# Optimization experiments

Hardware: AMD Instinct MI355X
Metric: run time of the kernel (lower is better)

## Reference

```python
import jax, jax.numpy as jnp
import numpy as np

V, D, H, L, T, B = 50257, 768, 12, 12, 1024, 2
S = 0.02


def setup_inputs() -> dict:
    key = jax.random.key(0)
    ks = jax.random.split(key, 8)
    return {
        "idx": jax.random.randint(ks[0], (B, T), 0, V),
        "wte": jax.random.normal(ks[1], (V, D), jnp.float32) * S,   # tied tok_emb / head
        "pos": jax.random.normal(ks[2], (T, D), jnp.float32) * S,
        "ln1_g": jnp.ones((L, D), jnp.float32),
        "ln1_b": jnp.zeros((L, D), jnp.float32),
        "qkv_w": jax.random.normal(ks[3], (L, D, 3 * D), jnp.float32) * S,
        "qkv_b": jnp.zeros((L, 3 * D), jnp.float32),
        "proj_w": jax.random.normal(ks[4], (L, D, D), jnp.float32) * S,
        "proj_b": jnp.zeros((L, D), jnp.float32),
        "ln2_g": jnp.ones((L, D), jnp.float32),
        "ln2_b": jnp.zeros((L, D), jnp.float32),
        "fc1_w": jax.random.normal(ks[5], (L, D, 4 * D), jnp.float32) * S,
        "fc1_b": jnp.zeros((L, 4 * D), jnp.float32),
        "fc2_w": jax.random.normal(ks[6], (L, 4 * D, D), jnp.float32) * S,
        "fc2_b": jnp.zeros((L, D), jnp.float32),
        "lnf_g": jnp.ones((D,), jnp.float32),
        "lnf_b": jnp.zeros((D,), jnp.float32),
    }


def _ln(x, g, b):
    m = x.mean(-1, keepdims=True)
    v = ((x - m) ** 2).mean(-1, keepdims=True)
    return (x - m) * jax.lax.rsqrt(v + 1e-5) * g + b


def reference(idx, wte, pos, ln1_g, ln1_b, qkv_w, qkv_b, proj_w, proj_b,
              ln2_g, ln2_b, fc1_w, fc1_b, fc2_w, fc2_b, lnf_g, lnf_b):
    b, t = idx.shape
    hd = D // H
    x = wte[idx] + pos[None, :t]                       # [B,T,D]
    causal = jnp.triu(jnp.ones((t, t), bool), 1)       # True above diagonal -> masked

    def block(x, p):
        l1g, l1b, qw, qb, pw, pb, l2g, l2b, f1w, f1b, f2w, f2b = p
        h = _ln(x, l1g, l1b)
        qkv = (h @ qw + qb).reshape(b, t, 3, H, hd).transpose(2, 0, 3, 1, 4)
        q, k, v = qkv[0], qkv[1], qkv[2]               # [B,H,T,hd]
        att = jnp.einsum('bhqd,bhkd->bhqk', q, k) * hd ** -0.5
        att = jnp.where(causal, -jnp.inf, att)
        att = jax.nn.softmax(att, axis=-1)
        o = jnp.einsum('bhqk,bhkd->bhqd', att, v)
        o = o.transpose(0, 2, 1, 3).reshape(b, t, D)
        x = x + o @ pw + pb
        h = _ln(x, l2g, l2b)
        h = jax.nn.gelu(h @ f1w + f1b, approximate=False)
        x = x + h @ f2w + f2b
        return x, None

    x, _ = jax.lax.scan(block, x, (ln1_g, ln1_b, qkv_w, qkv_b, proj_w, proj_b,
                                   ln2_g, ln2_b, fc1_w, fc1_b, fc2_w, fc2_b))
    x = _ln(x, lnf_g, lnf_b)
    return x @ wte.T                                   # tied head -> [B,T,V]
```

## Files before the change

kernel.cpp:

```cpp
#include <hip/hip_runtime.h>
#include <math.h>

#define D 768
#define T 1024
#define BATCH 2
#define NH 12
#define NL 12
#define V 50257
#define NT 2048

typedef _Float16 half4_t __attribute__((ext_vector_type(4)));
typedef _Float16 half8_t __attribute__((ext_vector_type(8)));
typedef float floatx4 __attribute__((ext_vector_type(4)));

__device__ inline float wave_reduce_sum(float v) {
  #pragma unroll
  for (int off = 32; off > 0; off >>= 1) v += __shfl_xor(v, off, 64);
  return v;
}

__device__ __forceinline__ void gld16(const _Float16* g, _Float16* l) {
  __builtin_amdgcn_global_load_lds(
      (const __attribute__((address_space(1))) unsigned int*)g,
      (__attribute__((address_space(3))) unsigned int*)l, 16, 0, 0);
}

__global__ __launch_bounds__(256) void embed_kernel(const int* __restrict__ idx,
    const float* __restrict__ wte, const float* __restrict__ pos,
    float* __restrict__ x) {
  int row = blockIdx.x;
  int tok = idx[row];
  int tp  = row & (T - 1);
  const float* ws = wte + (size_t)tok * D;
  const float* ps = pos + (size_t)tp * D;
  float* xr = x + (size_t)row * D;
  for (int i = threadIdx.x; i < D; i += 256) xr[i] = ws[i] + ps[i];
}

__global__ __launch_bounds__(256) void cvt16_kernel(const float* __restrict__ src,
    _Float16* __restrict__ dst, int n4) {
  int i = blockIdx.x * 256 + threadIdx.x;
  int stride = gridDim.x * 256;
  for (; i < n4; i += stride) {
    float4 v = ((const float4*)src)[i];
    half4_t h;
    h[0] = (_Float16)v.x; h[1] = (_Float16)v.y;
    h[2] = (_Float16)v.z; h[3] = (_Float16)v.w;
    ((half4_t*)dst)[i] = h;
  }
}

__global__ __launch_bounds__(256) void wconv_kernel(
    const float* __restrict__ qkvw, const float* __restrict__ projw,
    const float* __restrict__ fc1w, const float* __restrict__ fc2w,
    _Float16* __restrict__ q16, _Float16* __restrict__ p16,
    _Float16* __restrict__ f116, _Float16* __restrict__ f216) {
  int id = blockIdx.x;
  size_t l = blockIdx.y;
  const float* src; _Float16* dst; int K, N, tn;
  if (id < 1728)      { src = qkvw + l * (D * 3 * D); dst = q16  + l * (2304 * 768); K = 768;  N = 2304; tn = id; }
  else if (id < 2304) { src = projw + l * (D * D);    dst = p16  + l * (768 * 768);  K = 768;  N = 768;  tn = id - 1728; }
  else if (id < 4608) { src = fc1w + l * (D * 4 * D); dst = f116 + l * (3072 * 768); K = 768;  N = 3072; tn = id - 2304; }
  else                { src = fc2w + l * (4 * D * D); dst = f216 + l * (3072 * 768); K = 3072; N = 768;  tn = id - 4608; }
  int ntn = N >> 5;
  int tc = (tn % ntn) * 32;
  int tr = (tn / ntn) * 32;
  __shared__ float tile[32][33];
  int tx = threadIdx.x & 31, ty = threadIdx.x >> 5;
  #pragma unroll
  for (int j = 0; j < 4; ++j)
    tile[ty + 8 * j][tx] = src[(size_t)(tr + ty + 8 * j) * N + tc + tx];
  __syncthreads();
  #pragma unroll
  for (int j = 0; j < 4; ++j)
    dst[(size_t)(tc + ty + 8 * j) * K + tr + tx] = (_Float16)tile[tx][ty + 8 * j];
}

__global__ __launch_bounds__(256) void ln_kernel(const float* __restrict__ x,
    const float* __restrict__ g, const float* __restrict__ bta,
    _Float16* __restrict__ y) {
  const int lane = threadIdx.x & 63, wave = threadIdx.x >> 6;
  const int row = blockIdx.x * 4 + wave;
  const float4* xr = (const float4*)(x + (size_t)row * D);
  half4_t* yr = (half4_t*)(y + (size_t)row * D);

  float4 a[3];
  #pragma unroll
  for (int j = 0; j < 3; ++j) a[j] = xr[lane + 64 * j];

  float s = 0.f;
  #pragma unroll
  for (int j = 0; j < 3; ++j) s += a[j].x + a[j].y + a[j].z + a[j].w;
  float mean = wave_reduce_sum(s) * (1.f / D);

  float v = 0.f;
  #pragma unroll
  for (int j = 0; j < 3; ++j) {
    float dx = a[j].x - mean, dy = a[j].y - mean, dz = a[j].z - mean, dw = a[j].w - mean;
    v += dx * dx + dy * dy + dz * dz + dw * dw;
  }
  float rstd = rsqrtf(wave_reduce_sum(v) * (1.f / D) + 1e-5f);

  #pragma unroll
  for (int j = 0; j < 3; ++j) {
    float4 gg = ((const float4*)g)[lane + 64 * j];
    float4 bb = ((const float4*)bta)[lane + 64 * j];
    half4_t h;
    h[0] = (_Float16)((a[j].x - mean) * rstd * gg.x + bb.x);
    h[1] = (_Float16)((a[j].y - mean) * rstd * gg.y + bb.y);
    h[2] = (_Float16)((a[j].z - mean) * rstd * gg.z + bb.z);
    h[3] = (_Float16)((a[j].w - mean) * rstd * gg.w + bb.w);
    yr[lane + 64 * j] = h;
  }
}

__global__ __launch_bounds__(256) void attn_kernel(
    const _Float16* __restrict__ qkv,
    const _Float16* __restrict__ vt,
    _Float16* __restrict__ o) {
  const int qt   = (int)gridDim.x - 1 - (int)blockIdx.x;
  const int h    = blockIdx.y;
  const int b    = blockIdx.z;
  const int tid  = threadIdx.x;
  const int lane = tid & 63, wave = tid >> 6;
  const int lr = lane & 15, g = lane >> 4;
  const int lk = g * 8;
  const int cr = g * 4;

  __shared__ __align__(16) _Float16 Ks[2][2][64][32];
  __shared__ __align__(16) _Float16 Vs[2][2][64][32];
  __shared__ __align__(16) _Float16 Pl[4][16][72];

  const int RS = 3 * D;
  const int q0 = qt * 64 + wave * 16;

  const _Float16* qrow = qkv + (size_t)(b * T + q0 + lr) * RS + h * 64;
  half8_t aq0 = *(const half8_t*)(qrow + lk);
  half8_t aq1 = *(const half8_t*)(qrow + 32 + lk);
  #pragma unroll
  for (int j = 0; j < 8; ++j) { aq0[j] *= (_Float16)0.125f; aq1[j] *= (_Float16)0.125f; }

  const int sr = wave * 16 + (lane >> 2);
  const int sc = (lane & 3) * 8;
  const _Float16* ksrc = qkv + (size_t)(b * T + sr) * RS + D + h * 64 + sc;
  const _Float16* vsrc = vt + (size_t)((b * NH + h) * 64 + sr) * T + sc;

#define ASTAGE(bufn, kk) do {                                   \
    const _Float16* kp_ = ksrc + (size_t)((kk) * 64) * RS;      \
    gld16(kp_,      &Ks[bufn][0][wave * 16][0]);                \
    gld16(kp_ + 32, &Ks[bufn][1][wave * 16][0]);                \
    gld16(vsrc + (kk) * 64,      &Vs[bufn][0][wave * 16][0]);   \
    gld16(vsrc + (kk) * 64 + 32, &Vs[bufn][1][wave * 16][0]);   \
  } while (0)

  floatx4 oa[4] = {};
  float m_r[4] = {-1e30f, -1e30f, -1e30f, -1e30f};
  float l_r[4] = {0.f, 0.f, 0.f, 0.f};

  ASTAGE(0, 0);
  __syncthreads();

  for (int kt = 0; kt <= qt; ++kt) {
    const int cur = kt & 1;
    if (kt < qt) ASTAGE(cur ^ 1, kt + 1);

    floatx4 s4[4];
    #pragma unroll
    for (int kc = 0; kc < 4; ++kc) {
      half8_t bk0 = *(const half8_t*)&Ks[cur][0][kc * 16 + lr][lk];
      half8_t bk1 = *(const half8_t*)&Ks[cur][1][kc * 16 + lr][lk];
      floatx4 z = {};
      z = __builtin_amdgcn_mfma_f32_16x16x32_f16(aq0, bk0, z, 0, 0, 0);
      z = __builtin_amdgcn_mfma_f32_16x16x32_f16(aq1, bk1, z, 0, 0, 0);
      s4[kc] = z;
    }
    if (kt == qt) {
      #pragma unroll
      for (int kc = 0; kc < 4; ++kc)
        #pragma unroll
        for (int i = 0; i < 4; ++i)
          if (kc * 16 + lr > wave * 16 + cr + i) s4[kc][i] = -1e30f;
    }

    float alpha[4], psum[4];
    #pragma unroll
    for (int i = 0; i < 4; ++i) {
      float v = fmaxf(fmaxf(s4[0][i], s4[1][i]), fmaxf(s4[2][i], s4[3][i]));
      #pragma unroll
      for (int off = 1; off < 16; off <<= 1) v = fmaxf(v, __shfl_xor(v, off, 64));
      float mn = fmaxf(m_r[i], v);
      alpha[i] = __expf(m_r[i] - mn);
      m_r[i] = mn;
      psum[i] = 0.f;
    }
    #pragma unroll
    for (int kc = 0; kc < 4; ++kc)
      #pragma unroll
      for (int i = 0; i < 4; ++i) {
        float p = __expf(s4[kc][i] - m_r[i]);
        psum[i] += p;
        Pl[wave][cr + i][kc * 16 + lr] = (_Float16)p;
      }
    #pragma unroll
    for (int i = 0; i < 4; ++i) {
      float s = psum[i];
      #pragma unroll
      for (int off = 1; off < 16; off <<= 1) s += __shfl_xor(s, off, 64);
      l_r[i] = l_r[i] * alpha[i] + s;
    }
    #pragma unroll
    for (int dc = 0; dc < 4; ++dc)
      #pragma unroll
      for (int i = 0; i < 4; ++i) oa[dc][i] *= alpha[i];

    half8_t ap0 = *(const half8_t*)&Pl[wave][lr][lk];
    half8_t ap1 = *(const half8_t*)&Pl[wave][lr][32 + lk];
    #pragma unroll
    for (int dc = 0; dc < 4; ++dc) {
      half8_t bv0 = *(const half8_t*)&Vs[cur][0][dc * 16 + lr][lk];
      half8_t bv1 = *(const half8_t*)&Vs[cur][1][dc * 16 + lr][lk];
      oa[dc] = __builtin_amdgcn_mfma_f32_16x16x32_f16(ap0, bv0, oa[dc], 0, 0, 0);
      oa[dc] = __builtin_amdgcn_mfma_f32_16x16x32_f16(ap1, bv1, oa[dc], 0, 0, 0);
    }
    __syncthreads();
  }
#undef ASTAGE

  _Float16* orow = o + (size_t)(b * T + q0) * D + h * 64;
  #pragma unroll
  for (int i = 0; i < 4; ++i) {
    float inv = 1.f / l_r[i];
    #pragma unroll
    for (int dc = 0; dc < 4; ++dc)
      orow[(size_t)(cr + i) * D + dc * 16 + lr] = (_Float16)(oa[dc][i] * inv);
  }
}

template <bool GELU, bool VT, bool ATOMIC, bool NTS, typename OutT>
__global__ __launch_bounds__(256) void gemm16_kernel(
    const _Float16* __restrict__ A, const _Float16* __restrict__ Bt,
    const float* __restrict__ bias, const float* __restrict__ res,
    OutT* __restrict__ C, _Float16* __restrict__ vt, int M, int N, int K) {
  __shared__ __align__(16) char smem_raw[33792];
  _Float16 (*As)[128][32] = (_Float16(*)[128][32])smem_raw;
  _Float16 (*Bs)[128][32] = (_Float16(*)[128][32])(smem_raw + 16384);

  const int t = threadIdx.x;
  const int lane = t & 63, wave = t >> 6;

  const int gx = gridDim.x, gy = gridDim.y;
  const int nwg = gx * gy;
  int f = blockIdx.y * gx + blockIdx.x;
  int id = (f & 7) * (nwg >> 3) + (f >> 3);
  const int n0 = (id / gy) * 128;
  const int m0 = (id % gy) * 128;

  const int ks = K / gridDim.z;
  const int kbeg = blockIdx.z * ks, kend = kbeg + ks;

  const int wm = (wave >> 1) * 64, wn = (wave & 1) * 64;
  const int lr = lane & 15;
  const int lk = (lane >> 4) * 8;

  const int srow = lane >> 2;
  const int scol = (lane & 3) * 8;
  const _Float16* a_src0 = A + (size_t)(m0 + wave * 32 + srow) * K + scol;
  const _Float16* a_src1 = a_src0 + (size_t)16 * K;
  const int bn0 = min(n0 + wave * 32 + srow, N - 1);
  const int bn1 = min(n0 + wave * 32 + 16 + srow, N - 1);
  const _Float16* b_src0 = Bt + (size_t)bn0 * K + scol;
  const _Float16* b_src1 = Bt + (size_t)bn1 * K + scol;

#define GSTAGE(bufn, kk) do {                            \
    gld16(a_src0 + (kk), &As[bufn][wave * 32][0]);       \
    gld16(a_src1 + (kk), &As[bufn][wave * 32 + 16][0]);  \
    gld16(b_src0 + (kk), &Bs[bufn][wave * 32][0]);       \
    gld16(b_src1 + (kk), &Bs[bufn][wave * 32 + 16][0]);  \
  } while (0)

  floatx4 acc[4][4] = {};

  GSTAGE(0, kbeg);
  __syncthreads();

  const int nIter = (kend - kbeg) >> 5;
  for (int i = 0; i < nIter; ++i) {
    const int cur = i & 1;
    if (i + 1 < nIter) GSTAGE(cur ^ 1, kbeg + ((i + 1) << 5));

    half8_t af[4], bb[4];
    #pragma unroll
    for (int mi = 0; mi < 4; ++mi)
      af[mi] = *(const half8_t*)&As[cur][wm + mi * 16 + lr][lk];
    #pragma unroll
    for (int ni = 0; ni < 4; ++ni)
      bb[ni] = *(const half8_t*)&Bs[cur][wn + ni * 16 + lr][lk];
    #pragma unroll
    for (int mi = 0; mi < 4; ++mi)
      #pragma unroll
      for (int ni = 0; ni < 4; ++ni)
        acc[mi][ni] = __builtin_amdgcn_mfma_f32_16x16x32_f16(
            af[mi], bb[ni], acc[mi][ni], 0, 0, 0);
    __syncthreads();
  }
#undef GSTAGE

  const int cr = (lane >> 4) * 4;

  if (NTS) {
    float (*ob)[132] = (float(*)[132])smem_raw;
    #pragma unroll
    for (int h2 = 0; h2 < 2; ++h2) {
      __syncthreads();
      if ((wave >> 1) == h2) {
        #pragma unroll
        for (int mi = 0; mi < 4; ++mi)
          #pragma unroll
          for (int ni = 0; ni < 4; ++ni) {
            floatx4 v = acc[mi][ni];
            #pragma unroll
            for (int i = 0; i < 4; ++i)
              ob[mi * 16 + cr + i][wn + ni * 16 + lr] = v[i];
          }
      }
      __syncthreads();
      const int col = t & 127;
      const int n = n0 + col;
      if (n < N) {
        #pragma unroll
        for (int r2 = 0; r2 < 32; ++r2) {
          int rloc = r2 * 2 + (t >> 7);
          int m = m0 + h2 * 64 + rloc;
          __builtin_nontemporal_store((OutT)ob[rloc][col], &C[(size_t)m * N + n]);
        }
      }
    }
    return;
  }

  #pragma unroll
  for (int mi = 0; mi < 4; ++mi) {
    #pragma unroll
    for (int ni = 0; ni < 4; ++ni) {
      int n = n0 + wn + ni * 16 + lr;
      if (n >= N) continue;
      floatx4 v = acc[mi][ni];
      float bs = (bias && (!ATOMIC || blockIdx.z == 0)) ? bias[n] : 0.f;
      if (VT && n >= 2 * D) {
        int d  = n - 2 * D;
        int mb = m0 + wm + mi * 16 + cr;
        half4_t h4;
        #pragma unroll
        for (int i = 0; i < 4; ++i) h4[i] = (_Float16)(v[i] + bs);
        *(half4_t*)(vt + ((size_t)((mb >> 10) * NH + (d >> 6)) * 64 + (d & 63)) * T
                       + (mb & 1023)) = h4;
      } else if (ATOMIC) {
        #pragma unroll
        for (int i = 0; i < 4; ++i) {
          int m = m0 + wm + mi * 16 + cr + i;
          atomicAdd((float*)&C[(size_t)m * N + n], v[i] + bs);
        }
      } else {
        #pragma unroll
        for (int i = 0; i < 4; ++i) {
          int m = m0 + wm + mi * 16 + cr + i;
          float vv = v[i] + bs;
          if (res)  vv += res[(size_t)m * N + n];
          if (GELU) vv = 0.5f * vv * (1.f + erff(vv * 0.70710678118f));
          C[(size_t)m * N + n] = (OutT)vv;
        }
      }
    }
  }
}

extern "C" void kernel_launch(void* const* d_in, const int* in_sizes, int n_in,
                              void* d_out, int out_size, void* d_ws, size_t ws_size,
                              hipStream_t stream) {
  const int*   idx   = (const int*)d_in[0];
  const float* wte   = (const float*)d_in[1];
  const float* pos   = (const float*)d_in[2];
  const float* ln1g  = (const float*)d_in[3];
  const float* ln1b  = (const float*)d_in[4];
  const float* qkvw  = (const float*)d_in[5];
  const float* qkvb  = (const float*)d_in[6];
  const float* projw = (const float*)d_in[7];
  const float* projb = (const float*)d_in[8];
  const float* ln2g  = (const float*)d_in[9];
  const float* ln2b  = (const float*)d_in[10];
  const float* fc1w  = (const float*)d_in[11];
  const float* fc1b  = (const float*)d_in[12];
  const float* fc2w  = (const float*)d_in[13];
  const float* fc2b  = (const float*)d_in[14];
  const float* lnfg  = (const float*)d_in[15];
  const float* lnfb  = (const float*)d_in[16];
  float* out = (float*)d_out;

  float* ws = (float*)d_ws;
  float* x = ws;
  _Float16* big16  = (_Float16*)(x + (size_t)NT * D);
  _Float16* vt16   = big16 + (size_t)NT * 4 * D;
  _Float16* hbuf16 = vt16 + (size_t)BATCH * NH * 64 * T;
  _Float16* obuf16 = hbuf16 + (size_t)NT * D;
  _Float16* wte16  = obuf16 + (size_t)NT * D;
  _Float16* wbase  = wte16 + (size_t)V * D;

  const size_t QSZ = (size_t)2304 * 768, PSZ = (size_t)768 * 768;
  const size_t F1SZ = (size_t)3072 * 768, F2SZ = (size_t)3072 * 768;
  const size_t PERL = QSZ + PSZ + F1SZ + F2SZ;
  const size_t fixed_bytes = (char*)wbase - (char*)d_ws;
  const bool all12 = ws_size >= fixed_bytes + 12 * PERL * sizeof(_Float16);
  const int nlw = all12 ? 12 : 1;

  _Float16* q16  = wbase;
  _Float16* p16  = q16  + QSZ * nlw;
  _Float16* f116 = p16  + PSZ * nlw;
  _Float16* f216 = f116 + F1SZ * nlw;

  cvt16_kernel<<<2048, 256, 0, stream>>>(wte, wte16, (V * D) / 4);
  embed_kernel<<<NT, 256, 0, stream>>>(idx, wte, pos, x);
  if (all12)
    wconv_kernel<<<dim3(6912, 12), 256, 0, stream>>>(
        qkvw, projw, fc1w, fc2w, q16, p16, f116, f216);

  for (int l = 0; l < NL; ++l) {
    size_t lw = all12 ? (size_t)l : 0;
    if (!all12)
      wconv_kernel<<<dim3(6912, 1), 256, 0, stream>>>(
          qkvw + (size_t)l * D * 3 * D, projw + (size_t)l * D * D,
          fc1w + (size_t)l * D * 4 * D, fc2w + (size_t)l * 4 * D * D,
          q16, p16, f116, f216);
    ln_kernel<<<NT / 4, 256, 0, stream>>>(x, ln1g + (size_t)l * D, ln1b + (size_t)l * D, hbuf16);
    gemm16_kernel<false, true, false, false, _Float16><<<dim3(18, 16), 256, 0, stream>>>(
        hbuf16, q16 + lw * QSZ, qkvb + (size_t)l * 3 * D, nullptr, big16, vt16, NT, 3 * D, D);
    attn_kernel<<<dim3(T / 64, NH, BATCH), 256, 0, stream>>>(big16, vt16, obuf16);
    gemm16_kernel<false, false, true, false, float><<<dim3(6, 16, 2), 256, 0, stream>>>(
        obuf16, p16 + lw * PSZ, projb + (size_t)l * D, nullptr, x, nullptr, NT, D, D);
    ln_kernel<<<NT / 4, 256, 0, stream>>>(x, ln2g + (size_t)l * D, ln2b + (size_t)l * D, hbuf16);
    gemm16_kernel<true, false, false, false, _Float16><<<dim3(24, 16), 256, 0, stream>>>(
        hbuf16, f116 + lw * F1SZ, fc1b + (size_t)l * 4 * D, nullptr, big16, nullptr, NT, 4 * D, D);
    gemm16_kernel<false, false, true, false, float><<<dim3(6, 16, 4), 256, 0, stream>>>(
        big16, f216 + lw * F2SZ, fc2b + (size_t)l * D, nullptr, x, nullptr, NT, D, 4 * D);
  }

  ln_kernel<<<NT / 4, 256, 0, stream>>>(x, lnfg, lnfb, hbuf16);
  gemm16_kernel<false, false, false, true, float><<<dim3((V + 127) / 128, 16), 256, 0, stream>>>(
      hbuf16, wte16, nullptr, nullptr, out, nullptr, NT, V, D);
}
```

Baseline: 2.775 ms.

## Triple-buffer GEMM with vmcnt waits and use 256-row tiles for LM head

Moves the fp16 GEMM from double to triple buffering, issuing loads two stages ahead. The full __syncthreads is replaced by explicit s_waitcnt vmcnt counts plus raw barriers, so loads for later stages can stay in flight across iterations. The GEMM is also templated on the M tile: the vocab head GEMM now runs 512-thread blocks with 256x128 tiles, which halves the re-reads of wte. The cost is more LDS per block, which can lower occupancy, and hand-counted vmcnt values that must match the number of loads issued per stage.

```diff
diff --git a/kernel.cpp b/kernel.cpp
--- a/kernel.cpp
+++ b/kernel.cpp
@@ -23,6 +23,18 @@
   __builtin_amdgcn_global_load_lds(
       (const __attribute__((address_space(1))) unsigned int*)g,
       (__attribute__((address_space(3))) unsigned int*)l, 16, 0, 0);
+}
+
+template <int N> __device__ __forceinline__ void waitvm() {
+  if constexpr (N == 8)      asm volatile("s_waitcnt vmcnt(8)" ::: "memory");
+  else if constexpr (N == 7) asm volatile("s_waitcnt vmcnt(7)" ::: "memory");
+  else if constexpr (N == 6) asm volatile("s_waitcnt vmcnt(6)" ::: "memory");
+  else if constexpr (N == 5) asm volatile("s_waitcnt vmcnt(5)" ::: "memory");
+  else if constexpr (N == 4) asm volatile("s_waitcnt vmcnt(4)" ::: "memory");
+  else if constexpr (N == 3) asm volatile("s_waitcnt vmcnt(3)" ::: "memory");
+  else if constexpr (N == 2) asm volatile("s_waitcnt vmcnt(2)" ::: "memory");
+  else if constexpr (N == 1) asm volatile("s_waitcnt vmcnt(1)" ::: "memory");
+  else                       asm volatile("s_waitcnt vmcnt(0)" ::: "memory");
 }
 
 __global__ __launch_bounds__(256) void embed_kernel(const int* __restrict__ idx,
@@ -236,14 +248,17 @@
   }
 }
 
-template <bool GELU, bool VT, bool ATOMIC, bool NTS, typename OutT>
-__global__ __launch_bounds__(256) void gemm16_kernel(
+template <int BM, bool GELU, bool VT, bool ATOMIC, bool NTS, typename OutT>
+__global__ __launch_bounds__(2 * BM) void gemm16_kernel(
     const _Float16* __restrict__ A, const _Float16* __restrict__ Bt,
     const float* __restrict__ bias, const float* __restrict__ res,
     OutT* __restrict__ C, _Float16* __restrict__ vt, int M, int N, int K) {
-  __shared__ __align__(16) char smem_raw[33792];
-  _Float16 (*As)[128][32] = (_Float16(*)[128][32])smem_raw;
-  _Float16 (*Bs)[128][32] = (_Float16(*)[128][32])(smem_raw + 16384);
+  constexpr int LPS = (BM == 128) ? 4 : 3;
+  constexpr int ABYTES = BM * 32 * 2;
+  constexpr int BBYTES = 128 * 32 * 2;
+  __shared__ __align__(16) char smem_raw[3 * (ABYTES + BBYTES)];
+  auto As = (_Float16(*)[BM][32])smem_raw;
+  auto Bs = (_Float16(*)[128][32])(smem_raw + 3 * ABYTES);
 
   const int t = threadIdx.x;
   const int lane = t & 63, wave = t >> 6;
@@ -253,7 +268,7 @@
   int f = blockIdx.y * gx + blockIdx.x;
   int id = (f & 7) * (nwg >> 3) + (f >> 3);
   const int n0 = (id / gy) * 128;
-  const int m0 = (id % gy) * 128;
+  const int m0 = (id % gy) * BM;
 
   const int ks = K / gridDim.z;
   const int kbeg = blockIdx.z * ks, kend = kbeg + ks;
@@ -266,27 +281,37 @@
   const int scol = (lane & 3) * 8;
   const _Float16* a_src0 = A + (size_t)(m0 + wave * 32 + srow) * K + scol;
   const _Float16* a_src1 = a_src0 + (size_t)16 * K;
-  const int bn0 = min(n0 + wave * 32 + srow, N - 1);
-  const int bn1 = min(n0 + wave * 32 + 16 + srow, N - 1);
+  const int brow = (BM == 128) ? wave * 32 : wave * 16;
+  const int bn0 = min(n0 + brow + srow, N - 1);
+  const int bn1 = min(n0 + brow + 16 + srow, N - 1);
   const _Float16* b_src0 = Bt + (size_t)bn0 * K + scol;
   const _Float16* b_src1 = Bt + (size_t)bn1 * K + scol;
 
-#define GSTAGE(bufn, kk) do {                            \
-    gld16(a_src0 + (kk), &As[bufn][wave * 32][0]);       \
-    gld16(a_src1 + (kk), &As[bufn][wave * 32 + 16][0]);  \
-    gld16(b_src0 + (kk), &Bs[bufn][wave * 32][0]);       \
-    gld16(b_src1 + (kk), &Bs[bufn][wave * 32 + 16][0]);  \
-  } while (0)
+  auto GSTAGE = [&](int s, int kk) {
+    gld16(a_src0 + kk, &As[s][wave * 32][0]);
+    gld16(a_src1 + kk, &As[s][wave * 32 + 16][0]);
+    if constexpr (BM == 128) {
+      gld16(b_src0 + kk, &Bs[s][wave * 32][0]);
+      gld16(b_src1 + kk, &Bs[s][wave * 32 + 16][0]);
+    } else {
+      gld16(b_src0 + kk, &Bs[s][wave * 16][0]);
+    }
+  };
 
   floatx4 acc[4][4] = {};
+  const int nIter = (kend - kbeg) >> 5;
 
   GSTAGE(0, kbeg);
-  __syncthreads();
-
-  const int nIter = (kend - kbeg) >> 5;
+  if (nIter > 1) GSTAGE(1, kbeg + 32);
+
+  int cur = 0, nxt = 2;
   for (int i = 0; i < nIter; ++i) {
-    const int cur = i & 1;
-    if (i + 1 < nIter) GSTAGE(cur ^ 1, kbeg + ((i + 1) << 5));
+    const int rem = nIter - 1 - i;
+    if (rem >= 2) { GSTAGE(nxt, kbeg + ((i + 2) << 5)); waitvm<2 * LPS>(); }
+    else if (rem == 1) waitvm<LPS>();
+    else waitvm<0>();
+    __builtin_amdgcn_s_barrier();
+    __builtin_amdgcn_sched_barrier(0);
 
     half8_t af[4], bb[4];
     #pragma unroll
@@ -301,16 +326,22 @@
       for (int ni = 0; ni < 4; ++ni)
         acc[mi][ni] = __builtin_amdgcn_mfma_f32_16x16x32_f16(
             af[mi], bb[ni], acc[mi][ni], 0, 0, 0);
-    __syncthreads();
-  }
-#undef GSTAGE
+
+    __builtin_amdgcn_sched_barrier(0);
+    __builtin_amdgcn_s_barrier();
+    __builtin_amdgcn_sched_barrier(0);
+    cur = (cur == 2) ? 0 : cur + 1;
+    nxt = (nxt == 2) ? 0 : nxt + 1;
+  }
 
   const int cr = (lane >> 4) * 4;
 
-  if (NTS) {
+  if constexpr (NTS) {
+    constexpr int THREADS = 2 * BM;
+    constexpr int RPP = THREADS / 128;
     float (*ob)[132] = (float(*)[132])smem_raw;
     #pragma unroll
-    for (int h2 = 0; h2 < 2; ++h2) {
+    for (int h2 = 0; h2 < BM / 64; ++h2) {
       __syncthreads();
       if ((wave >> 1) == h2) {
         #pragma unroll
@@ -325,11 +356,12 @@
       }
       __syncthreads();
       const int col = t & 127;
+      const int rbase = t >> 7;
       const int n = n0 + col;
       if (n < N) {
         #pragma unroll
-        for (int r2 = 0; r2 < 32; ++r2) {
-          int rloc = r2 * 2 + (t >> 7);
+        for (int r2 = 0; r2 < 64 / RPP; ++r2) {
+          int rloc = r2 * RPP + rbase;
           int m = m0 + h2 * 64 + rloc;
           __builtin_nontemporal_store((OutT)ob[rloc][col], &C[(size_t)m * N + n]);
         }
@@ -431,19 +463,19 @@
           fc1w + (size_t)l * D * 4 * D, fc2w + (size_t)l * 4 * D * D,
           q16, p16, f116, f216);
     ln_kernel<<<NT / 4, 256, 0, stream>>>(x, ln1g + (size_t)l * D, ln1b + (size_t)l * D, hbuf16);
-    gemm16_kernel<false, true, false, false, _Float16><<<dim3(18, 16), 256, 0, stream>>>(
+    gemm16_kernel<128, false, true, false, false, _Float16><<<dim3(18, 16), 256, 0, stream>>>(
         hbuf16, q16 + lw * QSZ, qkvb + (size_t)l * 3 * D, nullptr, big16, vt16, NT, 3 * D, D);
     attn_kernel<<<dim3(T / 64, NH, BATCH), 256, 0, stream>>>(big16, vt16, obuf16);
-    gemm16_kernel<false, false, true, false, float><<<dim3(6, 16, 2), 256, 0, stream>>>(
+    gemm16_kernel<128, false, false, true, false, float><<<dim3(6, 16, 2), 256, 0, stream>>>(
         obuf16, p16 + lw * PSZ, projb + (size_t)l * D, nullptr, x, nullptr, NT, D, D);
     ln_kernel<<<NT / 4, 256, 0, stream>>>(x, ln2g + (size_t)l * D, ln2b + (size_t)l * D, hbuf16);
-    gemm16_kernel<true, false, false, false, _Float16><<<dim3(24, 16), 256, 0, stream>>>(
+    gemm16_kernel<128, true, false, false, false, _Float16><<<dim3(24, 16), 256, 0, stream>>>(
         hbuf16, f116 + lw * F1SZ, fc1b + (size_t)l * 4 * D, nullptr, big16, nullptr, NT, 4 * D, D);
-    gemm16_kernel<false, false, true, false, float><<<dim3(6, 16, 4), 256, 0, stream>>>(
+    gemm16_kernel<128, false, false, true, false, float><<<dim3(6, 16, 4), 256, 0, stream>>>(
         big16, f216 + lw * F2SZ, fc2b + (size_t)l * D, nullptr, x, nullptr, NT, D, 4 * D);
   }
 
   ln_kernel<<<NT / 4, 256, 0, stream>>>(x, lnfg, lnfb, hbuf16);
-  gemm16_kernel<false, false, false, true, float><<<dim3((V + 127) / 128, 16), 256, 0, stream>>>(
+  gemm16_kernel<256, false, false, false, true, float><<<dim3((V + 127) / 128, 8), 512, 0, stream>>>(
       hbuf16, wte16, nullptr, nullptr, out, nullptr, NT, V, D);
 }
```

After: 2.660 ms. 4.2% less time.
